# Kernel optimization log

Hardware: AMD Instinct MI355X
Metric: run time of the kernel (lower is better)

Reference implementation:

```python
import jax, jax.numpy as jnp
import numpy as np

EPS = 1e-5
N_LAYERS_TOTAL = 4  # n_layers + 1 convs


def setup_inputs() -> dict:
    key = jax.random.key(0)
    ks = jax.random.split(key, 6)
    B, N, C = 16, 2048, 128
    x = jax.random.normal(ks[0], (B, N, C), dtype=jnp.float32)
    adj = jax.random.uniform(ks[1], (B, N, N), dtype=jnp.float32)
    # per-layer params: weight [L,Cin,Cout], bias [L,Cout], bn gamma/beta [L,C]
    W = jax.random.normal(ks[2], (N_LAYERS_TOTAL, C, C), dtype=jnp.float32) * (1.0 / np.sqrt(C))
    b = jnp.zeros((N_LAYERS_TOTAL, C), dtype=jnp.float32)
    gamma = jnp.ones((N_LAYERS_TOTAL, C), dtype=jnp.float32)
    beta = jnp.zeros((N_LAYERS_TOTAL, C), dtype=jnp.float32)
    return {"x": x, "adj": adj, "W": W, "b": b, "gamma": gamma, "beta": beta}


def reference(x, adj, W, b, gamma, beta):
    # Stacked dense GCNConv -> ReLU -> BatchNorm1d (training mode).
    h = x
    for i in range(N_LAYERS_TOTAL):
        # GCNConv (dense, normalize=False): adj @ (h @ W) + b
        h = jnp.einsum('bnm,bmc->bnc', adj, h @ W[i]) + b[i]  # [B,N,C]
        h = jax.nn.relu(h)
        # BatchNorm over flattened (B*N) per channel, biased variance
        mu = jnp.mean(h, axis=(0, 1))
        var = jnp.mean(jnp.square(h - mu), axis=(0, 1))
        h = gamma[i] * (h - mu) * jax.lax.rsqrt(var + EPS) + beta[i]
    return h
```

## Files before the change

### kernel.cpp

```cpp
#include <hip/hip_runtime.h>
#include <stdint.h>
#include <stddef.h>

#define BATCH 16
#define NROW 2048
#define CH 128
#define NLAYER 4
#define NN_TOT (BATCH * NROW)
#define EPSV 1e-5f
#define KS 64
#define NKT (NROW / KS)

typedef short short8 __attribute__((ext_vector_type(8)));
typedef float f32x4 __attribute__((ext_vector_type(4)));

static __device__ __forceinline__ unsigned short f2bf(float f) {
  union { float f; unsigned int i; } v;
  v.f = f;
  unsigned int u = v.i;
  return (unsigned short)((u + 0x7FFFu + ((u >> 16) & 1u)) >> 16);
}
static __device__ __forceinline__ short8 pack8(const float* __restrict__ p) {
  f32x4 a = *(const f32x4*)p;
  f32x4 b = *(const f32x4*)(p + 4);
  short8 v;
  v[0] = (short)f2bf(a[0]); v[1] = (short)f2bf(a[1]);
  v[2] = (short)f2bf(a[2]); v[3] = (short)f2bf(a[3]);
  v[4] = (short)f2bf(b[0]); v[5] = (short)f2bf(b[1]);
  v[6] = (short)f2bf(b[2]); v[7] = (short)f2bf(b[3]);
  return v;
}

__global__ void prep_kernel(const float* __restrict__ Wl,
                            const float* __restrict__ gprev,
                            const float* __restrict__ bprev,
                            float* __restrict__ gsum, float* __restrict__ gsumsq,
                            unsigned short* __restrict__ Wt,
                            float* __restrict__ cvec,
                            float* __restrict__ sg, float* __restrict__ tg,
                            int first, int do_fold) {
  __shared__ float ss[CH], tt[CH];
  const int t = threadIdx.x;
  float s_, t_;
  if (first) {
    s_ = 1.0f; t_ = 0.0f;
  } else {
    const float inv = 1.0f / (float)NN_TOT;
    float mu = gsum[t] * inv;
    float var = gsumsq[t] * inv - mu * mu;
    s_ = gprev[t] * rsqrtf(var + EPSV);
    t_ = bprev[t] - mu * s_;
  }
  ss[t] = s_; tt[t] = t_;
  sg[t] = s_; tg[t] = t_;
  gsum[t] = 0.0f; gsumsq[t] = 0.0f;
  __syncthreads();
  if (do_fold) {
    float acc = 0.0f;
    for (int c = 0; c < CH; ++c) {
      float w = Wl[c * CH + t];
      acc += tt[c] * w;
      Wt[t * CH + c] = f2bf(ss[c] * w);
    }
    cvec[t] = acc;
  }
}

__global__ __launch_bounds__(256) void gemm1_kernel(
    const float* __restrict__ X,
    const unsigned short* __restrict__ Wt,
    const float* __restrict__ cvec,
    unsigned short* __restrict__ Yt) {
  __shared__ unsigned short As[64 * 128];
  __shared__ unsigned short Bs[128 * 128];
  const int tid = threadIdx.x;
  const int m0 = blockIdx.x * 64;

#pragma unroll
  for (int j = 0; j < 4; ++j) {
    int c = tid + 256 * j;
    int r = c >> 4, slot = c & 15;
    int kc = slot ^ (r & 15);
    *(short8*)(As + c * 8) = pack8(X + (size_t)(m0 + r) * CH + kc * 8);
  }
#pragma unroll
  for (int j = 0; j < 8; ++j) {
    int c = tid + 256 * j;
    int r = c >> 4, slot = c & 15;
    int kc = slot ^ (r & 15);
    *(short8*)(Bs + c * 8) = *(const short8*)(Wt + (size_t)r * CH + kc * 8);
  }
  __syncthreads();

  const int l = tid & 63, w = tid >> 6;
  const int mq = (w >> 1) * 32, oq = (w & 1) * 64;
  const int lr = l & 15, lq = l >> 4;
  f32x4 acc[2][4] = {};

#pragma unroll
  for (int kt = 0; kt < 4; ++kt) {
    const int kc0 = kt * 4 + lq;
    const int slotK = kc0 ^ lr;
    short8 a[2], b[4];
#pragma unroll
    for (int mi = 0; mi < 2; ++mi)
      a[mi] = *(const short8*)(As + (mq + mi * 16 + lr) * 128 + slotK * 8);
#pragma unroll
    for (int ni = 0; ni < 4; ++ni)
      b[ni] = *(const short8*)(Bs + (oq + ni * 16 + lr) * 128 + slotK * 8);
#pragma unroll
    for (int mi = 0; mi < 2; ++mi)
#pragma unroll
      for (int ni = 0; ni < 4; ++ni)
        acc[mi][ni] = __builtin_amdgcn_mfma_f32_16x16x32_bf16(a[mi], b[ni], acc[mi][ni], 0, 0, 0);
  }

  const int bat = m0 >> 11;
  const int mb = m0 & 2047;
  unsigned short* YtB = Yt + (size_t)bat * CH * NROW;
#pragma unroll
  for (int ni = 0; ni < 4; ++ni) {
    const int o = oq + ni * 16 + lr;
    const float cv = cvec[o];
    unsigned short* row = YtB + (size_t)o * NROW;
#pragma unroll
    for (int mi = 0; mi < 2; ++mi) {
      const int m = mb + mq + mi * 16 + lq * 4;
      f32x4 v = acc[mi][ni];
      unsigned short p0 = f2bf(v[0] + cv), p1 = f2bf(v[1] + cv);
      unsigned short p2 = f2bf(v[2] + cv), p3 = f2bf(v[3] + cv);
      unsigned long long packed = (unsigned long long)p0 | ((unsigned long long)p1 << 16) |
                                  ((unsigned long long)p2 << 32) | ((unsigned long long)p3 << 48);
      *(unsigned long long*)(row + m) = packed;
    }
  }
}

struct Pf {
  short8 a0, a1, a2, a3;
  short8 b0, b1;
  f32x4 f0, f1, f2, f3;
};

template <int CVT>
__global__ __launch_bounds__(256) void gemm2_kernel(
    const float* __restrict__ adjF,
    const unsigned short* __restrict__ adjH,
    unsigned short* __restrict__ adjO,
    const unsigned short* __restrict__ Yt,
    const float* __restrict__ bias,
    float* __restrict__ R,
    float* __restrict__ gsum, float* __restrict__ gsumsq) {
  __shared__ unsigned short As[2][CH * KS];
  __shared__ unsigned short Bs[2][64 * KS];
  __shared__ float redS[2][CH];
  __shared__ float redQ[2][CH];

  const int tid = threadIdx.x;
  const int bat = blockIdx.x >> 5;
  const int n0 = (blockIdx.x & 31) * 64;
  const unsigned short* YtB = Yt + (size_t)bat * CH * NROW;

  const int s8 = tid & 7;
  const int r8 = tid >> 3;
  const int swz8 = (s8 ^ (r8 & 7)) * 8;

  const unsigned short* gA0 = YtB + (size_t)r8 * NROW + s8 * 8;
  const unsigned short* gA1 = gA0 + (size_t)32 * NROW;
  const unsigned short* gA2 = gA0 + (size_t)64 * NROW;
  const unsigned short* gA3 = gA0 + (size_t)96 * NROW;
  const int lA0 = r8 * KS + swz8;
  const int lA1 = lA0 + 32 * KS;
  const int lA2 = lA0 + 64 * KS;
  const int lA3 = lA0 + 96 * KS;

  const size_t bO0 = (size_t)bat * NROW * NROW + (size_t)(n0 + r8) * NROW + s8 * 8;
  const size_t bO1 = bO0 + (size_t)32 * NROW;
  const int lB0 = r8 * KS + swz8;
  const int lB1 = lB0 + 32 * KS;

  const int l = tid & 63, w = tid >> 6;
  const int cq = (w >> 1) * 64;
  const int nh = (w & 1) * 32;
  const int lr = l & 15, lq = l >> 4;
  const int rsw = lr & 7;

  f32x4 acc[4][2] = {};

  auto LOADS = [&](Pf& p, int kt) {
    const int k0 = kt * KS;
    p.a0 = *(const short8*)(gA0 + k0);
    p.a1 = *(const short8*)(gA1 + k0);
    p.a2 = *(const short8*)(gA2 + k0);
    p.a3 = *(const short8*)(gA3 + k0);
    if constexpr (CVT) {
      const float* q0 = adjF + bO0 + k0;
      const float* q1 = adjF + bO1 + k0;
      p.f0 = *(const f32x4*)q0; p.f1 = *(const f32x4*)(q0 + 4);
      p.f2 = *(const f32x4*)q1; p.f3 = *(const f32x4*)(q1 + 4);
    } else {
      p.b0 = *(const short8*)(adjH + bO0 + k0);
      p.b1 = *(const short8*)(adjH + bO1 + k0);
    }
  };

  auto WRITES = [&](Pf& p, int buf, int kt) {
    unsigned short* Ap = As[buf];
    *(short8*)(Ap + lA0) = p.a0;
    *(short8*)(Ap + lA1) = p.a1;
    *(short8*)(Ap + lA2) = p.a2;
    *(short8*)(Ap + lA3) = p.a3;
    unsigned short* Bp = Bs[buf];
    if constexpr (CVT) {
      short8 q0, q1;
      q0[0] = (short)f2bf(p.f0[0]); q0[1] = (short)f2bf(p.f0[1]);
      q0[2] = (short)f2bf(p.f0[2]); q0[3] = (short)f2bf(p.f0[3]);
      q0[4] = (short)f2bf(p.f1[0]); q0[5] = (short)f2bf(p.f1[1]);
      q0[6] = (short)f2bf(p.f1[2]); q0[7] = (short)f2bf(p.f1[3]);
      q1[0] = (short)f2bf(p.f2[0]); q1[1] = (short)f2bf(p.f2[1]);
      q1[2] = (short)f2bf(p.f2[2]); q1[3] = (short)f2bf(p.f2[3]);
      q1[4] = (short)f2bf(p.f3[0]); q1[5] = (short)f2bf(p.f3[1]);
      q1[6] = (short)f2bf(p.f3[2]); q1[7] = (short)f2bf(p.f3[3]);
      *(short8*)(Bp + lB0) = q0;
      *(short8*)(Bp + lB1) = q1;
      const int k0 = kt * KS;
      *(short8*)(adjO + bO0 + k0) = q0;
      *(short8*)(adjO + bO1 + k0) = q1;
    } else {
      *(short8*)(Bp + lB0) = p.b0;
      *(short8*)(Bp + lB1) = p.b1;
    }
  };

  auto COMPUTE = [&](int buf) {
    const unsigned short* Ap = As[buf];
    const unsigned short* Bp = Bs[buf];
#pragma unroll
    for (int ks = 0; ks < 2; ++ks) {
      const int sl = ((ks * 4 + lq) ^ rsw) * 8;
      short8 a0 = *(const short8*)(Ap + (cq +  0 + lr) * KS + sl);
      short8 a1 = *(const short8*)(Ap + (cq + 16 + lr) * KS + sl);
      short8 a2 = *(const short8*)(Ap + (cq + 32 + lr) * KS + sl);
      short8 a3 = *(const short8*)(Ap + (cq + 48 + lr) * KS + sl);
      short8 b0 = *(const short8*)(Bp + (nh +  0 + lr) * KS + sl);
      short8 b1 = *(const short8*)(Bp + (nh + 16 + lr) * KS + sl);
      acc[0][0] = __builtin_amdgcn_mfma_f32_16x16x32_bf16(a0, b0, acc[0][0], 0, 0, 0);
      acc[0][1] = __builtin_amdgcn_mfma_f32_16x16x32_bf16(a0, b1, acc[0][1], 0, 0, 0);
      acc[1][0] = __builtin_amdgcn_mfma_f32_16x16x32_bf16(a1, b0, acc[1][0], 0, 0, 0);
      acc[1][1] = __builtin_amdgcn_mfma_f32_16x16x32_bf16(a1, b1, acc[1][1], 0, 0, 0);
      acc[2][0] = __builtin_amdgcn_mfma_f32_16x16x32_bf16(a2, b0, acc[2][0], 0, 0, 0);
      acc[2][1] = __builtin_amdgcn_mfma_f32_16x16x32_bf16(a2, b1, acc[2][1], 0, 0, 0);
      acc[3][0] = __builtin_amdgcn_mfma_f32_16x16x32_bf16(a3, b0, acc[3][0], 0, 0, 0);
      acc[3][1] = __builtin_amdgcn_mfma_f32_16x16x32_bf16(a3, b1, acc[3][1], 0, 0, 0);
    }
  };

#define BAR() do { asm volatile("s_waitcnt lgkmcnt(0)"); __builtin_amdgcn_s_barrier(); } while (0)

  Pf s0, s1;
  LOADS(s0, 0);
  WRITES(s0, 0, 0);
  LOADS(s0, 1);
  LOADS(s1, 2);
  BAR();

#pragma unroll 1
  for (int kt2 = 0; kt2 < 14; ++kt2) {
    const int kt = kt2 * 2;
    COMPUTE(0);
    WRITES(s0, 1, kt + 1);
    LOADS(s0, kt + 3);
    BAR();
    COMPUTE(1);
    WRITES(s1, 0, kt + 2);
    LOADS(s1, kt + 4);
    BAR();
  }
  COMPUTE(0);
  WRITES(s0, 1, 29);
  LOADS(s0, 31);
  BAR();
  COMPUTE(1);
  WRITES(s1, 0, 30);
  BAR();
  COMPUTE(0);
  WRITES(s0, 1, 31);
  BAR();
  COMPUTE(1);
#undef BAR

  float* RB = R + (size_t)bat * NROW * CH;
  f32x4 sumv[4] = {};
  f32x4 sumq[4] = {};
#pragma unroll
  for (int mi = 0; mi < 4; ++mi) {
    const int c0 = cq + mi * 16 + lq * 4;
    f32x4 bia = *(const f32x4*)(bias + c0);
#pragma unroll
    for (int ni = 0; ni < 2; ++ni) {
      const int n = n0 + nh + ni * 16 + lr;
      f32x4 v = acc[mi][ni] + bia;
      v[0] = fmaxf(v[0], 0.0f);
      v[1] = fmaxf(v[1], 0.0f);
      v[2] = fmaxf(v[2], 0.0f);
      v[3] = fmaxf(v[3], 0.0f);
      sumv[mi] += v;
      sumq[mi] += v * v;
      *(f32x4*)(RB + (size_t)n * CH + c0) = v;
    }
  }
#pragma unroll
  for (int mi = 0; mi < 4; ++mi) {
#pragma unroll
    for (int d = 1; d < 16; d <<= 1) {
      sumv[mi][0] += __shfl_xor(sumv[mi][0], d);
      sumv[mi][1] += __shfl_xor(sumv[mi][1], d);
      sumv[mi][2] += __shfl_xor(sumv[mi][2], d);
      sumv[mi][3] += __shfl_xor(sumv[mi][3], d);
      sumq[mi][0] += __shfl_xor(sumq[mi][0], d);
      sumq[mi][1] += __shfl_xor(sumq[mi][1], d);
      sumq[mi][2] += __shfl_xor(sumq[mi][2], d);
      sumq[mi][3] += __shfl_xor(sumq[mi][3], d);
    }
  }
  const int nqi = w & 1;
  if (lr == 0) {
#pragma unroll
    for (int mi = 0; mi < 4; ++mi) {
      const int c0 = cq + mi * 16 + lq * 4;
      redS[nqi][c0 + 0] = sumv[mi][0];
      redS[nqi][c0 + 1] = sumv[mi][1];
      redS[nqi][c0 + 2] = sumv[mi][2];
      redS[nqi][c0 + 3] = sumv[mi][3];
      redQ[nqi][c0 + 0] = sumq[mi][0];
      redQ[nqi][c0 + 1] = sumq[mi][1];
      redQ[nqi][c0 + 2] = sumq[mi][2];
      redQ[nqi][c0 + 3] = sumq[mi][3];
    }
  }
  __syncthreads();
  if (tid < CH) {
    atomicAdd(gsum + tid, redS[0][tid] + redS[1][tid]);
  } else {
    const int c = tid - CH;
    atomicAdd(gsumsq + c, redQ[0][c] + redQ[1][c]);
  }
}

__global__ void out_kernel(float* __restrict__ out,
                           const float* __restrict__ sg,
                           const float* __restrict__ tg) {
  const int total = NN_TOT * CH / 4;
  for (int idx = blockIdx.x * blockDim.x + threadIdx.x; idx < total;
       idx += gridDim.x * blockDim.x) {
    f32x4 v = *(f32x4*)(out + (size_t)idx * 4);
    const int c0 = (idx & 31) * 4;
    f32x4 s = *(const f32x4*)(sg + c0);
    f32x4 t = *(const f32x4*)(tg + c0);
    v = s * v + t;
    *(f32x4*)(out + (size_t)idx * 4) = v;
  }
}

extern "C" void kernel_launch(void* const* d_in, const int* in_sizes, int n_in,
                              void* d_out, int out_size, void* d_ws, size_t ws_size,
                              hipStream_t stream) {
  (void)in_sizes; (void)n_in; (void)out_size; (void)ws_size;
  const float* x     = (const float*)d_in[0];
  const float* adj   = (const float*)d_in[1];
  const float* W     = (const float*)d_in[2];
  const float* bvec  = (const float*)d_in[3];
  const float* gamma = (const float*)d_in[4];
  const float* beta  = (const float*)d_in[5];

  float* R = (float*)d_out;

  char* ws = (char*)d_ws;
  unsigned short* adjb = (unsigned short*)(ws);
  unsigned short* Yt   = (unsigned short*)(ws + 134217728);
  unsigned short* Wt   = (unsigned short*)(ws + 142606336);
  float* cvec   = (float*)(ws + 142606336 + 32768);
  float* sg     = (float*)(ws + 142606336 + 33280);
  float* tg     = (float*)(ws + 142606336 + 33792);
  float* gsum   = (float*)(ws + 142606336 + 34304);
  float* gsumsq = (float*)(ws + 142606336 + 34816);

  for (int i = 0; i < NLAYER; ++i) {
    prep_kernel<<<1, 128, 0, stream>>>(
        W + (size_t)i * CH * CH,
        gamma + (size_t)(i ? (i - 1) : 0) * CH, beta + (size_t)(i ? (i - 1) : 0) * CH,
        gsum, gsumsq, Wt, cvec, sg, tg, (i == 0) ? 1 : 0, 1);
    gemm1_kernel<<<512, 256, 0, stream>>>((i == 0) ? x : R, Wt, cvec, Yt);
    if (i == 0) {
      gemm2_kernel<1><<<512, 256, 0, stream>>>(adj, nullptr, adjb, Yt,
                                               bvec, R, gsum, gsumsq);
    } else {
      gemm2_kernel<0><<<512, 256, 0, stream>>>(nullptr, adjb, nullptr, Yt,
                                               bvec + (size_t)i * CH, R,
                                               gsum, gsumsq);
    }
  }
  prep_kernel<<<1, 128, 0, stream>>>(W, gamma + 3 * CH, beta + 3 * CH,
                                     gsum, gsumsq, Wt, cvec, sg, tg, 0, 0);
  out_kernel<<<512, 256, 0, stream>>>(R, sg, tg);
}
```

Measured before the change: 648.9 us.

## Fuse BN stats into gemm1/out kernels and load gemm2 A operand directly to registers

Drops the per-layer single-block prep kernels. All weights are transposed to bf16 once in an init kernel, and the BatchNorm scale/shift is computed inside gemm1 and applied to the input on load instead of being folded into W. Per-layer stat buffers replace the reset-each-layer scheme. In gemm2 the Yt (A) tile no longer goes through shared memory: each wave loads its A fragments straight from global into registers, double-buffered, which cuts LDS traffic and halves shared memory use. The cost is more redundant global reads of Yt across waves and higher register pressure.

```diff
diff --git a/kernel.cpp b/kernel.cpp
--- a/kernel.cpp
+++ b/kernel.cpp
@@ -9,7 +9,6 @@
 #define NN_TOT (BATCH * NROW)
 #define EPSV 1e-5f
 #define KS 64
-#define NKT (NROW / KS)
 
 typedef short short8 __attribute__((ext_vector_type(8)));
 typedef float f32x4 __attribute__((ext_vector_type(4)));
@@ -20,68 +19,71 @@
   unsigned int u = v.i;
   return (unsigned short)((u + 0x7FFFu + ((u >> 16) & 1u)) >> 16);
 }
-static __device__ __forceinline__ short8 pack8(const float* __restrict__ p) {
-  f32x4 a = *(const f32x4*)p;
-  f32x4 b = *(const f32x4*)(p + 4);
-  short8 v;
-  v[0] = (short)f2bf(a[0]); v[1] = (short)f2bf(a[1]);
-  v[2] = (short)f2bf(a[2]); v[3] = (short)f2bf(a[3]);
-  v[4] = (short)f2bf(b[0]); v[5] = (short)f2bf(b[1]);
-  v[6] = (short)f2bf(b[2]); v[7] = (short)f2bf(b[3]);
-  return v;
-}
-
-__global__ void prep_kernel(const float* __restrict__ Wl,
-                            const float* __restrict__ gprev,
-                            const float* __restrict__ bprev,
-                            float* __restrict__ gsum, float* __restrict__ gsumsq,
-                            unsigned short* __restrict__ Wt,
-                            float* __restrict__ cvec,
-                            float* __restrict__ sg, float* __restrict__ tg,
-                            int first, int do_fold) {
-  __shared__ float ss[CH], tt[CH];
+
+__global__ void init_kernel(const float* __restrict__ W,
+                            unsigned short* __restrict__ Wt4,
+                            float* __restrict__ gsum, float* __restrict__ gsumsq) {
+  const int l = blockIdx.x;
   const int t = threadIdx.x;
-  float s_, t_;
-  if (first) {
-    s_ = 1.0f; t_ = 0.0f;
-  } else {
-    const float inv = 1.0f / (float)NN_TOT;
-    float mu = gsum[t] * inv;
-    float var = gsumsq[t] * inv - mu * mu;
-    s_ = gprev[t] * rsqrtf(var + EPSV);
-    t_ = bprev[t] - mu * s_;
-  }
-  ss[t] = s_; tt[t] = t_;
-  sg[t] = s_; tg[t] = t_;
-  gsum[t] = 0.0f; gsumsq[t] = 0.0f;
-  __syncthreads();
-  if (do_fold) {
-    float acc = 0.0f;
-    for (int c = 0; c < CH; ++c) {
-      float w = Wl[c * CH + t];
-      acc += tt[c] * w;
-      Wt[t * CH + c] = f2bf(ss[c] * w);
-    }
-    cvec[t] = acc;
-  }
-}
-
+  const float* Wl = W + (size_t)l * CH * CH;
+  unsigned short* Wo = Wt4 + (size_t)l * CH * CH;
+  for (int idx = t; idx < CH * CH; idx += 256) {
+    int o = idx >> 7, c = idx & 127;
+    Wo[idx] = f2bf(Wl[c * CH + o]);
+  }
+  if (l == 0) {
+    for (int i = t; i < NLAYER * CH; i += 256) { gsum[i] = 0.0f; gsumsq[i] = 0.0f; }
+  }
+}
+
+template <int FIRST>
 __global__ __launch_bounds__(256) void gemm1_kernel(
     const float* __restrict__ X,
     const unsigned short* __restrict__ Wt,
-    const float* __restrict__ cvec,
+    const float* __restrict__ gp, const float* __restrict__ bp,
+    const float* __restrict__ gsumP, const float* __restrict__ gsumsqP,
     unsigned short* __restrict__ Yt) {
   __shared__ unsigned short As[64 * 128];
   __shared__ unsigned short Bs[128 * 128];
+  __shared__ __align__(16) float ss[CH];
+  __shared__ __align__(16) float tt[CH];
   const int tid = threadIdx.x;
   const int m0 = blockIdx.x * 64;
+
+  if (!FIRST) {
+    if (tid < CH) {
+      const float inv = 1.0f / (float)NN_TOT;
+      float mu = gsumP[tid] * inv;
+      float var = gsumsqP[tid] * inv - mu * mu;
+      float s_ = gp[tid] * rsqrtf(var + EPSV);
+      ss[tid] = s_;
+      tt[tid] = bp[tid] - mu * s_;
+    }
+    __syncthreads();
+  }
 
 #pragma unroll
   for (int j = 0; j < 4; ++j) {
     int c = tid + 256 * j;
     int r = c >> 4, slot = c & 15;
     int kc = slot ^ (r & 15);
-    *(short8*)(As + c * 8) = pack8(X + (size_t)(m0 + r) * CH + kc * 8);
+    const float* p = X + (size_t)(m0 + r) * CH + kc * 8;
+    f32x4 a = *(const f32x4*)p;
+    f32x4 b = *(const f32x4*)(p + 4);
+    if (!FIRST) {
+      f32x4 sa = *(const f32x4*)(ss + kc * 8);
+      f32x4 sb = *(const f32x4*)(ss + kc * 8 + 4);
+      f32x4 ta = *(const f32x4*)(tt + kc * 8);
+      f32x4 tb = *(const f32x4*)(tt + kc * 8 + 4);
+      a = sa * a + ta;
+      b = sb * b + tb;
+    }
+    short8 v;
+    v[0] = (short)f2bf(a[0]); v[1] = (short)f2bf(a[1]);
+    v[2] = (short)f2bf(a[2]); v[3] = (short)f2bf(a[3]);
+    v[4] = (short)f2bf(b[0]); v[5] = (short)f2bf(b[1]);
+    v[6] = (short)f2bf(b[2]); v[7] = (short)f2bf(b[3]);
+    *(short8*)(As + c * 8) = v;
   }
 #pragma unroll
   for (int j = 0; j < 8; ++j) {
@@ -121,14 +123,13 @@
 #pragma unroll
   for (int ni = 0; ni < 4; ++ni) {
     const int o = oq + ni * 16 + lr;
-    const float cv = cvec[o];
     unsigned short* row = YtB + (size_t)o * NROW;
 #pragma unroll
     for (int mi = 0; mi < 2; ++mi) {
       const int m = mb + mq + mi * 16 + lq * 4;
       f32x4 v = acc[mi][ni];
-      unsigned short p0 = f2bf(v[0] + cv), p1 = f2bf(v[1] + cv);
-      unsigned short p2 = f2bf(v[2] + cv), p3 = f2bf(v[3] + cv);
+      unsigned short p0 = f2bf(v[0]), p1 = f2bf(v[1]);
+      unsigned short p2 = f2bf(v[2]), p3 = f2bf(v[3]);
       unsigned long long packed = (unsigned long long)p0 | ((unsigned long long)p1 << 16) |
                                   ((unsigned long long)p2 << 32) | ((unsigned long long)p3 << 48);
       *(unsigned long long*)(row + m) = packed;
@@ -137,7 +138,6 @@
 }
 
 struct Pf {
-  short8 a0, a1, a2, a3;
   short8 b0, b1;
   f32x4 f0, f1, f2, f3;
 };
@@ -150,8 +150,7 @@
     const unsigned short* __restrict__ Yt,
     const float* __restrict__ bias,
     float* __restrict__ R,
-    float* __restrict__ gsum, float* __restrict__ gsumsq) {
-  __shared__ unsigned short As[2][CH * KS];
+    float* __restrict__ gsumL, float* __restrict__ gsumsqL) {
   __shared__ unsigned short Bs[2][64 * KS];
   __shared__ float redS[2][CH];
   __shared__ float redQ[2][CH];
@@ -164,16 +163,6 @@
   const int s8 = tid & 7;
   const int r8 = tid >> 3;
   const int swz8 = (s8 ^ (r8 & 7)) * 8;
-
-  const unsigned short* gA0 = YtB + (size_t)r8 * NROW + s8 * 8;
-  const unsigned short* gA1 = gA0 + (size_t)32 * NROW;
-  const unsigned short* gA2 = gA0 + (size_t)64 * NROW;
-  const unsigned short* gA3 = gA0 + (size_t)96 * NROW;
-  const int lA0 = r8 * KS + swz8;
-  const int lA1 = lA0 + 32 * KS;
-  const int lA2 = lA0 + 64 * KS;
-  const int lA3 = lA0 + 96 * KS;
-
   const size_t bO0 = (size_t)bat * NROW * NROW + (size_t)(n0 + r8) * NROW + s8 * 8;
   const size_t bO1 = bO0 + (size_t)32 * NROW;
   const int lB0 = r8 * KS + swz8;
@@ -185,14 +174,12 @@
   const int lr = l & 15, lq = l >> 4;
   const int rsw = lr & 7;
 
+  const unsigned short* aBase = YtB + (size_t)(cq + lr) * NROW + lq * 8;
+
   f32x4 acc[4][2] = {};
 
-  auto LOADS = [&](Pf& p, int kt) {
+  auto LOADB = [&](Pf& p, int kt) {
     const int k0 = kt * KS;
-    p.a0 = *(const short8*)(gA0 + k0);
-    p.a1 = *(const short8*)(gA1 + k0);
-    p.a2 = *(const short8*)(gA2 + k0);
-    p.a3 = *(const short8*)(gA3 + k0);
     if constexpr (CVT) {
       const float* q0 = adjF + bO0 + k0;
       const float* q1 = adjF + bO1 + k0;
@@ -204,12 +191,7 @@
     }
   };
 
-  auto WRITES = [&](Pf& p, int buf, int kt) {
-    unsigned short* Ap = As[buf];
-    *(short8*)(Ap + lA0) = p.a0;
-    *(short8*)(Ap + lA1) = p.a1;
-    *(short8*)(Ap + lA2) = p.a2;
-    *(short8*)(Ap + lA3) = p.a3;
+  auto WRITEB = [&](Pf& p, int buf, int kt) {
     unsigned short* Bp = Bs[buf];
     if constexpr (CVT) {
       short8 q0, q1;
@@ -232,61 +214,69 @@
     }
   };
 
-  auto COMPUTE = [&](int buf) {
-    const unsigned short* Ap = As[buf];
+  auto LOADA = [&](short8* ar, int kt) {
+    const int k0 = kt * KS;
+#pragma unroll
+    for (int mi = 0; mi < 4; ++mi)
+#pragma unroll
+      for (int ks = 0; ks < 2; ++ks)
+        ar[mi * 2 + ks] = *(const short8*)(aBase + (size_t)mi * 16 * NROW + k0 + ks * 32);
+  };
+
+  auto COMPUTE = [&](int buf, const short8* ar) {
     const unsigned short* Bp = Bs[buf];
 #pragma unroll
     for (int ks = 0; ks < 2; ++ks) {
       const int sl = ((ks * 4 + lq) ^ rsw) * 8;
-      short8 a0 = *(const short8*)(Ap + (cq +  0 + lr) * KS + sl);
-      short8 a1 = *(const short8*)(Ap + (cq + 16 + lr) * KS + sl);
-      short8 a2 = *(const short8*)(Ap + (cq + 32 + lr) * KS + sl);
-      short8 a3 = *(const short8*)(Ap + (cq + 48 + lr) * KS + sl);
-      short8 b0 = *(const short8*)(Bp + (nh +  0 + lr) * KS + sl);
+      short8 b0 = *(const short8*)(Bp + (nh + 0 + lr) * KS + sl);
       short8 b1 = *(const short8*)(Bp + (nh + 16 + lr) * KS + sl);
-      acc[0][0] = __builtin_amdgcn_mfma_f32_16x16x32_bf16(a0, b0, acc[0][0], 0, 0, 0);
-      acc[0][1] = __builtin_amdgcn_mfma_f32_16x16x32_bf16(a0, b1, acc[0][1], 0, 0, 0);
-      acc[1][0] = __builtin_amdgcn_mfma_f32_16x16x32_bf16(a1, b0, acc[1][0], 0, 0, 0);
-      acc[1][1] = __builtin_amdgcn_mfma_f32_16x16x32_bf16(a1, b1, acc[1][1], 0, 0, 0);
-      acc[2][0] = __builtin_amdgcn_mfma_f32_16x16x32_bf16(a2, b0, acc[2][0], 0, 0, 0);
-      acc[2][1] = __builtin_amdgcn_mfma_f32_16x16x32_bf16(a2, b1, acc[2][1], 0, 0, 0);
-      acc[3][0] = __builtin_amdgcn_mfma_f32_16x16x32_bf16(a3, b0, acc[3][0], 0, 0, 0);
-      acc[3][1] = __builtin_amdgcn_mfma_f32_16x16x32_bf16(a3, b1, acc[3][1], 0, 0, 0);
+#pragma unroll
+      for (int mi = 0; mi < 4; ++mi) {
+        acc[mi][0] = __builtin_amdgcn_mfma_f32_16x16x32_bf16(ar[mi * 2 + ks], b0, acc[mi][0], 0, 0, 0);
+        acc[mi][1] = __builtin_amdgcn_mfma_f32_16x16x32_bf16(ar[mi * 2 + ks], b1, acc[mi][1], 0, 0, 0);
+      }
     }
   };
 
 #define BAR() do { asm volatile("s_waitcnt lgkmcnt(0)"); __builtin_amdgcn_s_barrier(); } while (0)
 
   Pf s0, s1;
-  LOADS(s0, 0);
-  WRITES(s0, 0, 0);
-  LOADS(s0, 1);
-  LOADS(s1, 2);
+  short8 arX[8], arY[8];
+  LOADB(s0, 0);
+  LOADA(arX, 0);
+  WRITEB(s0, 0, 0);
+  LOADB(s0, 1);
+  LOADB(s1, 2);
   BAR();
 
 #pragma unroll 1
   for (int kt2 = 0; kt2 < 14; ++kt2) {
     const int kt = kt2 * 2;
-    COMPUTE(0);
-    WRITES(s0, 1, kt + 1);
-    LOADS(s0, kt + 3);
+    LOADA(arY, kt + 1);
+    WRITEB(s0, 1, kt + 1);
+    LOADB(s0, kt + 3);
+    COMPUTE(0, arX);
     BAR();
-    COMPUTE(1);
-    WRITES(s1, 0, kt + 2);
-    LOADS(s1, kt + 4);
+    LOADA(arX, kt + 2);
+    WRITEB(s1, 0, kt + 2);
+    LOADB(s1, kt + 4);
+    COMPUTE(1, arY);
     BAR();
   }
-  COMPUTE(0);
-  WRITES(s0, 1, 29);
-  LOADS(s0, 31);
+  LOADA(arY, 29);
+  WRITEB(s0, 1, 29);
+  LOADB(s0, 31);
+  COMPUTE(0, arX);
   BAR();
-  COMPUTE(1);
-  WRITES(s1, 0, 30);
+  LOADA(arX, 30);
+  WRITEB(s1, 0, 30);
+  COMPUTE(1, arY);
   BAR();
-  COMPUTE(0);
-  WRITES(s0, 1, 31);
+  LOADA(arY, 31);
+  WRITEB(s0, 1, 31);
+  COMPUTE(0, arX);
   BAR();
-  COMPUTE(1);
+  COMPUTE(1, arY);
 #undef BAR
 
   float* RB = R + (size_t)bat * NROW * CH;
@@ -340,23 +330,35 @@
   }
   __syncthreads();
   if (tid < CH) {
-    atomicAdd(gsum + tid, redS[0][tid] + redS[1][tid]);
+    atomicAdd(gsumL + tid, redS[0][tid] + redS[1][tid]);
   } else {
     const int c = tid - CH;
-    atomicAdd(gsumsq + c, redQ[0][c] + redQ[1][c]);
-  }
-}
-
-__global__ void out_kernel(float* __restrict__ out,
-                           const float* __restrict__ sg,
-                           const float* __restrict__ tg) {
+    atomicAdd(gsumsqL + c, redQ[0][c] + redQ[1][c]);
+  }
+}
+
+__global__ __launch_bounds__(256) void out_kernel(
+    float* __restrict__ out,
+    const float* __restrict__ g3, const float* __restrict__ b3,
+    const float* __restrict__ gsum3, const float* __restrict__ gsumsq3) {
+  __shared__ __align__(16) float ss[CH];
+  __shared__ __align__(16) float tt[CH];
+  if (threadIdx.x < CH) {
+    const float inv = 1.0f / (float)NN_TOT;
+    float mu = gsum3[threadIdx.x] * inv;
+    float var = gsumsq3[threadIdx.x] * inv - mu * mu;
+    float s_ = g3[threadIdx.x] * rsqrtf(var + EPSV);
+    ss[threadIdx.x] = s_;
+    tt[threadIdx.x] = b3[threadIdx.x] - mu * s_;
+  }
+  __syncthreads();
   const int total = NN_TOT * CH / 4;
   for (int idx = blockIdx.x * blockDim.x + threadIdx.x; idx < total;
        idx += gridDim.x * blockDim.x) {
     f32x4 v = *(f32x4*)(out + (size_t)idx * 4);
     const int c0 = (idx & 31) * 4;
-    f32x4 s = *(const f32x4*)(sg + c0);
-    f32x4 t = *(const f32x4*)(tg + c0);
+    f32x4 s = *(const f32x4*)(ss + c0);
+    f32x4 t = *(const f32x4*)(tt + c0);
     v = s * v + t;
     *(f32x4*)(out + (size_t)idx * 4) = v;
   }
@@ -378,29 +380,28 @@
   char* ws = (char*)d_ws;
   unsigned short* adjb = (unsigned short*)(ws);
   unsigned short* Yt   = (unsigned short*)(ws + 134217728);
-  unsigned short* Wt   = (unsigned short*)(ws + 142606336);
-  float* cvec   = (float*)(ws + 142606336 + 32768);
-  float* sg     = (float*)(ws + 142606336 + 33280);
-  float* tg     = (float*)(ws + 142606336 + 33792);
-  float* gsum   = (float*)(ws + 142606336 + 34304);
-  float* gsumsq = (float*)(ws + 142606336 + 34816);
+  unsigned short* Wt4  = (unsigned short*)(ws + 142606336);
+  float* gsum   = (float*)(ws + 142606336 + 131072);
+  float* gsumsq = (float*)(ws + 142606336 + 131072 + 2048);
+
+  init_kernel<<<4, 256, 0, stream>>>(W, Wt4, gsum, gsumsq);
 
   for (int i = 0; i < NLAYER; ++i) {
-    prep_kernel<<<1, 128, 0, stream>>>(
-        W + (size_t)i * CH * CH,
-        gamma + (size_t)(i ? (i - 1) : 0) * CH, beta + (size_t)(i ? (i - 1) : 0) * CH,
-        gsum, gsumsq, Wt, cvec, sg, tg, (i == 0) ? 1 : 0, 1);
-    gemm1_kernel<<<512, 256, 0, stream>>>((i == 0) ? x : R, Wt, cvec, Yt);
     if (i == 0) {
-      gemm2_kernel<1><<<512, 256, 0, stream>>>(adj, nullptr, adjb, Yt,
-                                               bvec, R, gsum, gsumsq);
+      gemm1_kernel<1><<<512, 256, 0, stream>>>(
+          x, Wt4, nullptr, nullptr, nullptr, nullptr, Yt);
+      gemm2_kernel<1><<<512, 256, 0, stream>>>(
+          adj, nullptr, adjb, Yt, bvec, R, gsum, gsumsq);
     } else {
-      gemm2_kernel<0><<<512, 256, 0, stream>>>(nullptr, adjb, nullptr, Yt,
-                                               bvec + (size_t)i * CH, R,
-                                               gsum, gsumsq);
-    }
-  }
-  prep_kernel<<<1, 128, 0, stream>>>(W, gamma + 3 * CH, beta + 3 * CH,
-                                     gsum, gsumsq, Wt, cvec, sg, tg, 0, 0);
-  out_kernel<<<512, 256, 0, stream>>>(R, sg, tg);
-}
+      gemm1_kernel<0><<<512, 256, 0, stream>>>(
+          R, Wt4 + (size_t)i * CH * CH,
+          gamma + (size_t)(i - 1) * CH, beta + (size_t)(i - 1) * CH,
+          gsum + (size_t)(i - 1) * CH, gsumsq + (size_t)(i - 1) * CH, Yt);
+      gemm2_kernel<0><<<512, 256, 0, stream>>>(
+          nullptr, adjb, nullptr, Yt, bvec + (size_t)i * CH, R,
+          gsum + (size_t)i * CH, gsumsq + (size_t)i * CH);
+    }
+  }
+  out_kernel<<<512, 256, 0, stream>>>(R, gamma + 3 * CH, beta + 3 * CH,
+                                      gsum + 3 * CH, gsumsq + 3 * CH);
+}
```

After: 684.0 us. 5.4% more time.
